# Kernel tuning notes

Hardware: AMD Instinct MI355X
Metric: run time of the kernel (lower is better)

## Reference

```python
import jax, jax.numpy as jnp
import numpy as np

DIM = 1024
HEADS = 8
NUM_EXPERTS = 65536
NUM_KEYS = 256  # sqrt(NUM_EXPERTS)
DIM_KEY = 512
TOPK = 16  # product_key_topk == num_experts_per_head


def setup_inputs() -> dict:
    key = jax.random.key(0)
    ks = jax.random.split(key, 6)
    B, N = 2, 512
    x = jax.random.normal(ks[0], (B, N, DIM), dtype=jnp.float32)
    gamma = jnp.ones((DIM,), dtype=jnp.float32)
    wq = jax.random.normal(ks[1], (2 * HEADS * DIM_KEY, DIM), dtype=jnp.float32) * 0.02
    keys = jax.random.normal(ks[2], (HEADS, NUM_KEYS, 2, DIM_KEY), dtype=jnp.float32) * 0.02
    table_down = jax.random.normal(ks[3], (NUM_EXPERTS, DIM), dtype=jnp.float32) * 0.02
    table_up = jax.random.normal(ks[4], (NUM_EXPERTS, DIM), dtype=jnp.float32) * 0.02
    return {"x": x, "gamma": gamma, "wq": wq, "keys": keys,
            "table_down": table_down, "table_up": table_up}


def _rmsnorm(v, g):
    # torch F.normalize(x, dim=-1) * gamma * sqrt(dim)
    scale = jnp.sqrt(jnp.asarray(v.shape[-1], v.dtype))
    n = jnp.maximum(jnp.linalg.norm(v, axis=-1, keepdims=True), 1e-12)
    return v / n * g * scale


def reference(x, gamma, wq, keys, table_down, table_up):
    B, N, D = x.shape
    xn = _rmsnorm(x, gamma)          # pre_rmsnorm on x
    gate = xn                        # x_in_gate is None -> gate = norm(x)
    # queries: b n (p h d) -> p b n h d
    q = gate @ wq.T                  # [B,N,2*H*DK]
    q = q.reshape(B, N, 2, HEADS, DIM_KEY).transpose(2, 0, 1, 3, 4)  # [2,B,N,H,DK]
    # sim: p b n h d, h k p d -> p b n h k
    sim = jnp.einsum('pbnhd,hkpd->pbnhk', q, keys)
    sx, ix = jax.lax.top_k(sim[0], TOPK)  # [B,N,H,TOPK]
    sy, iy = jax.lax.top_k(sim[1], TOPK)
    # outer sums over the two product-key axes -> [B,N,H,TOPK*TOPK]
    all_scores = (sx[..., :, None] + sy[..., None, :]).reshape(B, N, HEADS, TOPK * TOPK)
    all_indices = (ix[..., :, None] * NUM_KEYS + iy[..., None, :]).reshape(B, N, HEADS, TOPK * TOPK)
    scores, pk = jax.lax.top_k(all_scores, TOPK)           # [B,N,H,K]
    indices = jnp.take_along_axis(all_indices, pk, axis=-1)  # expert ids [B,N,H,K]
    wd = table_down[indices]  # [B,N,H,K,D]
    wu = table_up[indices]    # [B,N,H,K,D]
    h = jnp.einsum('bnd,bnhkd->bnhk', xn, wd)
    h = jax.nn.gelu(h, approximate=False) * jax.nn.softmax(scores, axis=-1)
    out = jnp.einsum('bnhk,bnhkd->bnd', h, wu)
    return out
```

## Files before the change

### kernel.cpp

```cpp
#include <hip/hip_runtime.h>
#include <math.h>


#define DIMV 1024

__global__ __launch_bounds__(256) void peer_rmsnorm(const float* __restrict__ x,
                                                    const float* __restrict__ gamma,
                                                    float* __restrict__ xnf)
{
    int t = blockIdx.x;
    int tid = threadIdx.x;
    const float4* xr = (const float4*)(x + (size_t)t * DIMV);
    float4 v = xr[tid];
    double ss = (double)v.x*v.x + (double)v.y*v.y + (double)v.z*v.z + (double)v.w*v.w;
    #pragma unroll
    for (int off = 32; off > 0; off >>= 1) ss += __shfl_xor(ss, off);
    __shared__ double red[4];
    if ((tid & 63) == 0) red[tid >> 6] = ss;
    __syncthreads();
    double tot = red[0] + red[1] + red[2] + red[3];
    float n32 = (float)fmax(sqrt(tot), 1e-12);
    const float4* g4 = (const float4*)gamma;
    float4 gv = g4[tid];
    float4 o;
    o.x = __fmul_rn(__fmul_rn(__fdiv_rn(v.x, n32), gv.x), 32.0f);
    o.y = __fmul_rn(__fmul_rn(__fdiv_rn(v.y, n32), gv.y), 32.0f);
    o.z = __fmul_rn(__fmul_rn(__fdiv_rn(v.z, n32), gv.z), 32.0f);
    o.w = __fmul_rn(__fmul_rn(__fdiv_rn(v.w, n32), gv.w), 32.0f);
    ((float4*)(xnf + (size_t)t * DIMV))[tid] = o;
}

__global__ __launch_bounds__(256) void peer_qgemm(const float* __restrict__ A,
                                                  const float* __restrict__ Bm,
                                                  float* __restrict__ C)
{
    int m0 = blockIdx.y * 128, n0 = blockIdx.x * 128;
    __shared__ float As[8][128];
    __shared__ float Bs[8][128];
    int tid = threadIdx.x;
    int tx = tid & 15, ty = tid >> 4;
    float acc[8][8] = {};
    int lrow = tid >> 1;
    int lk   = (tid & 1) * 4;
    for (int k0 = 0; k0 < 1024; k0 += 8) {
        float4 av = *(const float4*)(A + (long)(m0 + lrow) * 1024 + (k0 + lk));
        As[lk+0][lrow] = av.x; As[lk+1][lrow] = av.y;
        As[lk+2][lrow] = av.z; As[lk+3][lrow] = av.w;
        float4 bv = *(const float4*)(Bm + (long)(n0 + lrow) * 1024 + (k0 + lk));
        Bs[lk+0][lrow] = bv.x; Bs[lk+1][lrow] = bv.y;
        Bs[lk+2][lrow] = bv.z; Bs[lk+3][lrow] = bv.w;
        __syncthreads();
        #pragma unroll
        for (int kk = 0; kk < 8; kk++) {
            float4 a0 = *(const float4*)&As[kk][ty*8];
            float4 a1 = *(const float4*)&As[kk][ty*8+4];
            float4 b0 = *(const float4*)&Bs[kk][tx*8];
            float4 b1 = *(const float4*)&Bs[kk][tx*8+4];
            float ra[8] = {a0.x,a0.y,a0.z,a0.w,a1.x,a1.y,a1.z,a1.w};
            float rb[8] = {b0.x,b0.y,b0.z,b0.w,b1.x,b1.y,b1.z,b1.w};
            #pragma unroll
            for (int i = 0; i < 8; i++)
                #pragma unroll
                for (int j = 0; j < 8; j++)
                    acc[i][j] = __fmaf_rn(ra[i], rb[j], acc[i][j]);
        }
        __syncthreads();
    }
    #pragma unroll
    for (int i = 0; i < 8; i++) {
        float4 c0 = {acc[i][0], acc[i][1], acc[i][2], acc[i][3]};
        float4 c1 = {acc[i][4], acc[i][5], acc[i][6], acc[i][7]};
        *(float4*)(C + (long)(m0 + ty*8 + i) * 8192 + (n0 + tx*8)) = c0;
        *(float4*)(C + (long)(m0 + ty*8 + i) * 8192 + (n0 + tx*8 + 4)) = c1;
    }
}

__global__ __launch_bounds__(256) void peer_sim(const float* __restrict__ qf,
                                                const float* __restrict__ keys,
                                                float* __restrict__ simf)
{
    int tb = blockIdx.x;
    int z  = blockIdx.y;
    int h = z & 7, p = z >> 3;
    int tid = threadIdx.x;
    __shared__ float4 qs[8][128];
    int t0 = tb * 8;
    long qbase = (long)h * 512 + (long)p * 4096;
    int row = tid >> 5, c16 = (tid & 31) * 4;
    const float4* qrow = (const float4*)(qf + (long)(t0 + row) * 8192 + qbase);
    #pragma unroll
    for (int u = 0; u < 4; u++) qs[row][c16 + u] = qrow[c16 + u];
    __syncthreads();
    int k = tid;
    const float4* krow = (const float4*)(keys + (long)h * 262144 + (long)k * 1024 + (long)p * 512);
    float pa[8][4] = {};
    for (int d4 = 0; d4 < 128; d4++) {
        float4 kv = krow[d4];
        #pragma unroll
        for (int tt = 0; tt < 8; tt++) {
            float4 qv = qs[tt][d4];
            pa[tt][0] = __fadd_rn(pa[tt][0], __fmul_rn(qv.x, kv.x));
            pa[tt][1] = __fadd_rn(pa[tt][1], __fmul_rn(qv.y, kv.y));
            pa[tt][2] = __fadd_rn(pa[tt][2], __fmul_rn(qv.z, kv.z));
            pa[tt][3] = __fadd_rn(pa[tt][3], __fmul_rn(qv.w, kv.w));
        }
    }
    #pragma unroll
    for (int tt = 0; tt < 8; tt++) {
        float s = __fadd_rn(__fadd_rn(pa[tt][0], pa[tt][2]),
                            __fadd_rn(pa[tt][1], pa[tt][3]));
        simf[(long)(t0 + tt) * 4096 + (long)p * 2048 + h * 256 + k] = s;
    }
}

__device__ inline void peer_select16(float v[4], int lane, float* outv, int* outi)
{
    for (int iter = 0; iter < 16; iter++) {
        float bv = -INFINITY; int bk = 1 << 30;
        #pragma unroll
        for (int i = 0; i < 4; i++) {
            int k = i * 64 + lane;
            if (v[i] > bv || (v[i] == bv && k < bk)) { bv = v[i]; bk = k; }
        }
        #pragma unroll
        for (int off = 32; off > 0; off >>= 1) {
            float ov = __shfl_xor(bv, off);
            int   ok = __shfl_xor(bk, off);
            if (ov > bv || (ov == bv && ok < bk)) { bv = ov; bk = ok; }
        }
        if (lane == 0) { outv[iter] = bv; outi[iter] = bk; }
        __syncthreads();
        if ((bk & 63) == lane) v[bk >> 6] = -INFINITY;
    }
}

__global__ __launch_bounds__(64) void peer_topk(const float* __restrict__ sim,
                                                float* __restrict__ wsel,
                                                int* __restrict__ esel)
{
    int b = blockIdx.x;
    int t = b >> 3, h = b & 7;
    int lane = threadIdx.x;
    const float* simx = sim + (size_t)t * 4096 + h * 256;
    const float* simy = simx + 2048;
    __shared__ float sxv[16]; __shared__ int sxi[16];
    __shared__ float syv[16]; __shared__ int syi[16];
    __shared__ float cv[16];  __shared__ int cf[16];
    float v[4];
    #pragma unroll
    for (int i = 0; i < 4; i++) v[i] = simx[i*64 + lane];
    peer_select16(v, lane, sxv, sxi);
    __syncthreads();
    #pragma unroll
    for (int i = 0; i < 4; i++) v[i] = simy[i*64 + lane];
    peer_select16(v, lane, syv, syi);
    __syncthreads();
    #pragma unroll
    for (int i = 0; i < 4; i++) {
        int f = i*64 + lane;
        v[i] = __fadd_rn(sxv[f >> 4], syv[f & 15]);
    }
    peer_select16(v, lane, cv, cf);
    __syncthreads();
    double m = (double)cv[0];
    double w = (lane < 16) ? exp((double)cv[lane] - m) : 0.0;
    double Z = w;
    #pragma unroll
    for (int off = 32; off > 0; off >>= 1) Z += __shfl_xor(Z, off);
    if (lane < 16) {
        int f = cf[lane];
        esel[b * 16 + lane] = sxi[f >> 4] * 256 + syi[f & 15];
        wsel[b * 16 + lane] = (float)(w / Z);
    }
}

__global__ __launch_bounds__(256) void peer_down(const float* __restrict__ xn,
                                                 const float* __restrict__ table_down,
                                                 const int* __restrict__ esel,
                                                 const float* __restrict__ wsel,
                                                 float* __restrict__ g)
{
    int tid = threadIdx.x;
    int wv = (blockIdx.x << 2) | (tid >> 6);
    int lane = tid & 63;
    int t = wv >> 7;
    __shared__ float4 xs[256];
    xs[tid] = ((const float4*)(xn + (size_t)t * DIMV))[tid];
    __syncthreads();
    int e = esel[wv];
    const float4* dr = (const float4*)(table_down + (size_t)e * DIMV);
    double acc = 0.0;
    #pragma unroll
    for (int it = 0; it < 4; it++) {
        int d4 = it * 64 + lane;
        float4 a = xs[d4];
        float4 bb = dr[d4];
        acc = fma((double)a.x, (double)bb.x, acc);
        acc = fma((double)a.y, (double)bb.y, acc);
        acc = fma((double)a.z, (double)bb.z, acc);
        acc = fma((double)a.w, (double)bb.w, acc);
    }
    #pragma unroll
    for (int off = 32; off > 0; off >>= 1) acc += __shfl_xor(acc, off);
    if (lane == 0) {
        double hv = acc;
        double ge = 0.5 * hv * (1.0 + erf(hv * 0.70710678118654752));
        g[wv] = (float)(ge * (double)wsel[wv]);
    }
}

__global__ __launch_bounds__(256) void peer_up(const float* __restrict__ table_up,
                                               const int* __restrict__ esel,
                                               const float* __restrict__ gbuf,
                                               float* __restrict__ out)
{
    int t = blockIdx.x;
    int tid = threadIdx.x;
    __shared__ float gs[128];
    __shared__ int   es[128];
    if (tid < 128) { gs[tid] = gbuf[t * 128 + tid]; es[tid] = esel[t * 128 + tid]; }
    __syncthreads();
    double a0 = 0, a1 = 0, a2 = 0, a3 = 0;
    for (int j = 0; j < 128; j++) {
        const float4* up = (const float4*)(table_up + (size_t)es[j] * DIMV);
        double gj = (double)gs[j];
        float4 u = up[tid];
        a0 = fma(gj, (double)u.x, a0); a1 = fma(gj, (double)u.y, a1);
        a2 = fma(gj, (double)u.z, a2); a3 = fma(gj, (double)u.w, a3);
    }
    float4 o = {(float)a0, (float)a1, (float)a2, (float)a3};
    ((float4*)(out + (size_t)t * DIMV))[tid] = o;
}

extern "C" void kernel_launch(void* const* d_in, const int* in_sizes, int n_in,
                              void* d_out, int out_size, void* d_ws, size_t ws_size,
                              hipStream_t stream)
{
    const float* x          = (const float*)d_in[0];
    const float* gamma      = (const float*)d_in[1];
    const float* wq         = (const float*)d_in[2];
    const float* keys       = (const float*)d_in[3];
    const float* table_down = (const float*)d_in[4];
    const float* table_up   = (const float*)d_in[5];
    float* out = (float*)d_out;
    char* wsb  = (char*)d_ws;

    float* xnf  = (float*)(wsb);
    float* qf   = (float*)(wsb + (4ull<<20));
    float* simf = (float*)(wsb + (36ull<<20));
    float* wsel = (float*)(wsb + (52ull<<20));
    int*   esel = (int*)  (wsb + (52ull<<20) + (512ull<<10));
    float* g    = (float*)(wsb + (53ull<<20));
    if (ws_size < (54ull << 20)) return;

    peer_rmsnorm<<<1024, 256, 0, stream>>>(x, gamma, xnf);

    peer_qgemm<<<dim3(64, 8, 1), 256, 0, stream>>>(xnf, wq, qf);

    peer_sim<<<dim3(128, 16, 1), 256, 0, stream>>>(qf, keys, simf);

    peer_topk<<<8192, 64, 0, stream>>>(simf, wsel, esel);

    peer_down<<<32768, 256, 0, stream>>>(xnf, table_down, esel, wsel, g);

    peer_up<<<1024, 256, 0, stream>>>(table_up, esel, g, out);
}
```

Baseline: 610.2 us.

## Double-buffer qgemm with smaller M tile, widen sim tokens, split up-projection

The query GEMM now uses a 64x128 tile with double-buffered shared memory. Its shared-memory layout is padded to avoid bank conflicts, and each k-step's global loads are prefetched while the previous step computes. The sim kernel processes 16 tokens per block instead of 8, so each loaded key row is reused more often, at the cost of more registers. The up-projection is split into four 64-thread blocks per token, each covering a quarter of the output dimension, to raise parallelism. Together these aim to cut GEMM stalls, key reloads and up-projection latency.

```diff
diff --git a/kernel.cpp b/kernel.cpp
--- a/kernel.cpp
+++ b/kernel.cpp
@@ -34,44 +34,65 @@
                                                   const float* __restrict__ Bm,
                                                   float* __restrict__ C)
 {
-    int m0 = blockIdx.y * 128, n0 = blockIdx.x * 128;
-    __shared__ float As[8][128];
-    __shared__ float Bs[8][128];
-    int tid = threadIdx.x;
+    __shared__ float As[2][8][80];
+    __shared__ float Bs[2][8][160];
+    int tid = threadIdx.x;
+    int m0 = blockIdx.y * 64, n0 = blockIdx.x * 128;
     int tx = tid & 15, ty = tid >> 4;
-    float acc[8][8] = {};
-    int lrow = tid >> 1;
-    int lk   = (tid & 1) * 4;
+    int rb = tid >> 1, hb = (tid & 1) * 4;
+    int ra = rb & 63;
+    int ca = 5 * (ra >> 2) + (ra & 3);
+    int cb = 5 * (rb >> 2) + (rb & 3);
+    float acc[4][8] = {};
+    float4 av, bv;
+    if (tid < 128) av = *(const float4*)(A  + (long)(m0 + ra) * 1024 + hb);
+    bv = *(const float4*)(Bm + (long)(n0 + rb) * 1024 + hb);
+    if (tid < 128) {
+        #pragma unroll
+        for (int j = 0; j < 4; j++) As[0][hb + j][ca] = ((const float*)&av)[j];
+    }
+    #pragma unroll
+    for (int j = 0; j < 4; j++) Bs[0][hb + j][cb] = ((const float*)&bv)[j];
+    int cur = 0;
     for (int k0 = 0; k0 < 1024; k0 += 8) {
-        float4 av = *(const float4*)(A + (long)(m0 + lrow) * 1024 + (k0 + lk));
-        As[lk+0][lrow] = av.x; As[lk+1][lrow] = av.y;
-        As[lk+2][lrow] = av.z; As[lk+3][lrow] = av.w;
-        float4 bv = *(const float4*)(Bm + (long)(n0 + lrow) * 1024 + (k0 + lk));
-        Bs[lk+0][lrow] = bv.x; Bs[lk+1][lrow] = bv.y;
-        Bs[lk+2][lrow] = bv.z; Bs[lk+3][lrow] = bv.w;
         __syncthreads();
+        bool more = (k0 + 8) < 1024;
+        if (more) {
+            if (tid < 128) av = *(const float4*)(A  + (long)(m0 + ra) * 1024 + (k0 + 8 + hb));
+            bv = *(const float4*)(Bm + (long)(n0 + rb) * 1024 + (k0 + 8 + hb));
+        }
         #pragma unroll
         for (int kk = 0; kk < 8; kk++) {
-            float4 a0 = *(const float4*)&As[kk][ty*8];
-            float4 a1 = *(const float4*)&As[kk][ty*8+4];
-            float4 b0 = *(const float4*)&Bs[kk][tx*8];
-            float4 b1 = *(const float4*)&Bs[kk][tx*8+4];
-            float ra[8] = {a0.x,a0.y,a0.z,a0.w,a1.x,a1.y,a1.z,a1.w};
-            float rb[8] = {b0.x,b0.y,b0.z,b0.w,b1.x,b1.y,b1.z,b1.w};
+            float4 a0 = *(const float4*)&As[cur][kk][5 * ty];
+            float4 b0 = *(const float4*)&Bs[cur][kk][10 * tx];
+            float4 b1 = *(const float4*)&Bs[cur][kk][10 * tx + 5];
+            float ra4[4] = {a0.x, a0.y, a0.z, a0.w};
+            float rb8[8] = {b0.x, b0.y, b0.z, b0.w, b1.x, b1.y, b1.z, b1.w};
             #pragma unroll
-            for (int i = 0; i < 8; i++)
+            for (int i = 0; i < 4; i++)
                 #pragma unroll
                 for (int j = 0; j < 8; j++)
-                    acc[i][j] = __fmaf_rn(ra[i], rb[j], acc[i][j]);
+                    acc[i][j] = __fmaf_rn(ra4[i], rb8[j], acc[i][j]);
         }
         __syncthreads();
-    }
-    #pragma unroll
-    for (int i = 0; i < 8; i++) {
+        if (more) {
+            int nxt = cur ^ 1;
+            if (tid < 128) {
+                #pragma unroll
+                for (int j = 0; j < 4; j++) As[nxt][hb + j][ca] = ((const float*)&av)[j];
+            }
+            #pragma unroll
+            for (int j = 0; j < 4; j++) Bs[nxt][hb + j][cb] = ((const float*)&bv)[j];
+            cur = nxt;
+        }
+    }
+    #pragma unroll
+    for (int i = 0; i < 4; i++) {
         float4 c0 = {acc[i][0], acc[i][1], acc[i][2], acc[i][3]};
         float4 c1 = {acc[i][4], acc[i][5], acc[i][6], acc[i][7]};
-        *(float4*)(C + (long)(m0 + ty*8 + i) * 8192 + (n0 + tx*8)) = c0;
-        *(float4*)(C + (long)(m0 + ty*8 + i) * 8192 + (n0 + tx*8 + 4)) = c1;
+        long r = (long)(m0 + ty * 4 + i) * 8192 + (n0 + tx * 8);
+        *(float4*)(C + r)     = c0;
+        *(float4*)(C + r + 4) = c1;
     }
 }
 
@@ -83,21 +104,21 @@
     int z  = blockIdx.y;
     int h = z & 7, p = z >> 3;
     int tid = threadIdx.x;
-    __shared__ float4 qs[8][128];
-    int t0 = tb * 8;
+    __shared__ float4 qs[16][128];
+    int t0 = tb * 16;
     long qbase = (long)h * 512 + (long)p * 4096;
-    int row = tid >> 5, c16 = (tid & 31) * 4;
+    int row = tid >> 4, c0 = (tid & 15) * 8;
     const float4* qrow = (const float4*)(qf + (long)(t0 + row) * 8192 + qbase);
     #pragma unroll
-    for (int u = 0; u < 4; u++) qs[row][c16 + u] = qrow[c16 + u];
+    for (int u = 0; u < 8; u++) qs[row][c0 + u] = qrow[c0 + u];
     __syncthreads();
     int k = tid;
     const float4* krow = (const float4*)(keys + (long)h * 262144 + (long)k * 1024 + (long)p * 512);
-    float pa[8][4] = {};
+    float pa[16][4] = {};
     for (int d4 = 0; d4 < 128; d4++) {
         float4 kv = krow[d4];
         #pragma unroll
-        for (int tt = 0; tt < 8; tt++) {
+        for (int tt = 0; tt < 16; tt++) {
             float4 qv = qs[tt][d4];
             pa[tt][0] = __fadd_rn(pa[tt][0], __fmul_rn(qv.x, kv.x));
             pa[tt][1] = __fadd_rn(pa[tt][1], __fmul_rn(qv.y, kv.y));
@@ -106,7 +127,7 @@
         }
     }
     #pragma unroll
-    for (int tt = 0; tt < 8; tt++) {
+    for (int tt = 0; tt < 16; tt++) {
         float s = __fadd_rn(__fadd_rn(pa[tt][0], pa[tt][2]),
                             __fadd_rn(pa[tt][1], pa[tt][3]));
         simf[(long)(t0 + tt) * 4096 + (long)p * 2048 + h * 256 + k] = s;
@@ -209,27 +230,31 @@
     }
 }
 
-__global__ __launch_bounds__(256) void peer_up(const float* __restrict__ table_up,
-                                               const int* __restrict__ esel,
-                                               const float* __restrict__ gbuf,
-                                               float* __restrict__ out)
-{
-    int t = blockIdx.x;
-    int tid = threadIdx.x;
+__global__ __launch_bounds__(64) void peer_up(const float* __restrict__ table_up,
+                                              const int* __restrict__ esel,
+                                              const float* __restrict__ gbuf,
+                                              float* __restrict__ out)
+{
+    int t  = blockIdx.x >> 2;
+    int ds = blockIdx.x & 3;
+    int lane = threadIdx.x;
     __shared__ float gs[128];
     __shared__ int   es[128];
-    if (tid < 128) { gs[tid] = gbuf[t * 128 + tid]; es[tid] = esel[t * 128 + tid]; }
-    __syncthreads();
+    gs[lane]      = gbuf[t * 128 + lane];
+    gs[lane + 64] = gbuf[t * 128 + 64 + lane];
+    es[lane]      = esel[t * 128 + lane];
+    es[lane + 64] = esel[t * 128 + 64 + lane];
+    __syncthreads();
+    int dbase = ds * 256 + lane * 4;
     double a0 = 0, a1 = 0, a2 = 0, a3 = 0;
     for (int j = 0; j < 128; j++) {
-        const float4* up = (const float4*)(table_up + (size_t)es[j] * DIMV);
+        const float4 u = *(const float4*)(table_up + (size_t)es[j] * DIMV + dbase);
         double gj = (double)gs[j];
-        float4 u = up[tid];
         a0 = fma(gj, (double)u.x, a0); a1 = fma(gj, (double)u.y, a1);
         a2 = fma(gj, (double)u.z, a2); a3 = fma(gj, (double)u.w, a3);
     }
     float4 o = {(float)a0, (float)a1, (float)a2, (float)a3};
-    ((float4*)(out + (size_t)t * DIMV))[tid] = o;
+    *(float4*)(out + (size_t)t * DIMV + dbase) = o;
 }
 
 extern "C" void kernel_launch(void* const* d_in, const int* in_sizes, int n_in,
@@ -255,13 +280,13 @@
 
     peer_rmsnorm<<<1024, 256, 0, stream>>>(x, gamma, xnf);
 
-    peer_qgemm<<<dim3(64, 8, 1), 256, 0, stream>>>(xnf, wq, qf);
-
-    peer_sim<<<dim3(128, 16, 1), 256, 0, stream>>>(qf, keys, simf);
+    peer_qgemm<<<dim3(64, 16, 1), 256, 0, stream>>>(xnf, wq, qf);
+
+    peer_sim<<<dim3(64, 16, 1), 256, 0, stream>>>(qf, keys, simf);
 
     peer_topk<<<8192, 64, 0, stream>>>(simf, wsel, esel);
 
     peer_down<<<32768, 256, 0, stream>>>(xnf, table_down, esel, wsel, g);
 
-    peer_up<<<1024, 256, 0, stream>>>(table_up, esel, g, out);
-}
+    peer_up<<<4096, 64, 0, stream>>>(table_up, esel, g, out);
+}
```

After: 608.9 us. About the same (-0.2%).
